# Kernel tuning notes

Hardware: AMD Instinct MI355X
Metric: run time of the kernel (lower is better)

Reference implementation:

```python
import jax, jax.numpy as jnp
import numpy as np
from jax import lax

DIM = 192
HEADS = 6

def conv1x1(x, w, b):
    # x: [B,C,H,W], w: [O,C], b: [O]
    return jnp.einsum('oc,bchw->bohw', w, x) + b[None, :, None, None]

def dwconv3x3(x, w, b):
    # x: [B,C,H,W], w: [C,1,3,3] depthwise
    y = lax.conv_general_dilated(x, w, window_strides=(1, 1), padding='SAME',
                                 feature_group_count=x.shape[1],
                                 dimension_numbers=('NCHW', 'OIHW', 'NCHW'))
    return y + b[None, :, None, None]

def l2norm(x, eps=1e-12):
    # normalize along last axis (matches torch F.normalize)
    n = jnp.sqrt(jnp.sum(x * x, axis=-1, keepdims=True))
    return x / jnp.maximum(n, eps)

def setup_inputs() -> dict:
    key = jax.random.key(0)
    ks = jax.random.split(key, 12)
    b, c, h, w = 8, DIM, 128, 128
    s = 0.02
    return {
        'hsi': jax.random.normal(ks[0], (b, c, h, w), jnp.float32),
        'lidar': jax.random.normal(ks[1], (b, c, h, w), jnp.float32),
        'hsi_qv_w': jax.random.normal(ks[2], (2 * c, c), jnp.float32) * s,
        'hsi_qv_b': jnp.zeros((2 * c,), jnp.float32),
        'lidar_kv_w': jax.random.normal(ks[3], (2 * c, c), jnp.float32) * s,
        'lidar_kv_b': jnp.zeros((2 * c,), jnp.float32),
        'hsi_dw_w': jax.random.normal(ks[4], (2 * c, 1, 3, 3), jnp.float32) * s,
        'hsi_dw_b': jnp.zeros((2 * c,), jnp.float32),
        'lidar_dw_w': jax.random.normal(ks[5], (2 * c, 1, 3, 3), jnp.float32) * s,
        'lidar_dw_b': jnp.zeros((2 * c,), jnp.float32),
        'temperature': jnp.ones((HEADS, 1, 1), jnp.float32),
    }

def reference(hsi, lidar, hsi_qv_w, hsi_qv_b, lidar_kv_w, lidar_kv_b,
              hsi_dw_w, hsi_dw_b, lidar_dw_w, lidar_dw_b, temperature):
    b, c, h, w = hsi.shape
    hd = c // HEADS  # per-head channel dim
    hw = h * w

    hsi_qv = dwconv3x3(conv1x1(hsi, hsi_qv_w, hsi_qv_b), hsi_dw_w, hsi_dw_b)
    hsi_q, hsi_v = jnp.split(hsi_qv, 2, axis=1)
    lidar_kv = dwconv3x3(conv1x1(lidar, lidar_kv_w, lidar_kv_b), lidar_dw_w, lidar_dw_b)
    lidar_k, lidar_v = jnp.split(lidar_kv, 2, axis=1)

    def to_heads(x):  # [B,C,H,W] -> [B,head,hd,HW]
        return x.reshape(b, HEADS, hd, hw)

    q = l2norm(to_heads(hsi_q))
    k = l2norm(to_heads(lidar_k))
    v_h = to_heads(hsi_v)
    v_l = to_heads(lidar_v)

    attn = jnp.einsum('bncs,bnds->bncd', q, k) * temperature[None]  # [B,head,hd,hd]
    attn = jax.nn.softmax(attn, axis=-1)  # dropout is identity in eval mode

    hsi_out = jnp.einsum('bncd,bnds->bncs', attn, v_h) + v_h
    lidar_out = jnp.einsum('bncd,bnds->bncs', attn, v_l) + v_l

    hsi_out = hsi_out.reshape(b, c, h, w) + hsi
    lidar_out = lidar_out.reshape(b, c, h, w) + lidar
    return (hsi_out, lidar_out)
```

## Files before the change

kernel.cpp:

```cpp
#include <hip/hip_runtime.h>

typedef short v8s __attribute__((ext_vector_type(8)));
typedef float v4f __attribute__((ext_vector_type(4)));
typedef float v32f __attribute__((ext_vector_type(32)));

__device__ __forceinline__ unsigned short f2bf(float f){
  unsigned u = __builtin_bit_cast(unsigned, f);
  return (unsigned short)((u + 0x7fffu + ((u>>16)&1u)) >> 16);
}
__device__ __forceinline__ float bf2f(unsigned short s){
  return __builtin_bit_cast(float, ((unsigned)s) << 16);
}

__global__ __launch_bounds__(512) void k_conv1x1(
    const float* __restrict__ hsi, const float* __restrict__ lidar,
    const unsigned short* __restrict__ Wfrag, const float* __restrict__ hqb,
    const float* __restrict__ lkb, unsigned short* __restrict__ S)
{
  const int bx   = blockIdx.x;
  const int tens = bx >> 11;
  const int nt   = bx & 2047;
  const int b    = nt >> 8;
  const int hw0  = (nt & 255) << 6;
  const float* X = (tens ? lidar : hsi) + ((size_t)b * 192) * 16384 + hw0;
  const float* bias = tens ? lkb : hqb;
  unsigned short* sb = S + ((size_t)(tens*8 + b) * 384) * 16384 + hw0;

  __shared__ unsigned short Xt[64][200];

  {
    const int c4   = (threadIdx.x & 15) * 4;
    const int krow = threadIdx.x >> 4;
    const float* xb2 = X + c4;
    float4 f[6];
    #pragma unroll
    for (int j = 0; j < 3; ++j){
      const int k = krow*2 + j*64;
      f[2*j]   = *(const float4*)(xb2 + (size_t)k * 16384);
      f[2*j+1] = *(const float4*)(xb2 + (size_t)(k+1) * 16384);
    }
    #pragma unroll
    for (int j = 0; j < 3; ++j){
      const int k = krow*2 + j*64;
      #pragma unroll
      for (int i2 = 0; i2 < 4; ++i2){
        const unsigned lo = f2bf(((const float*)&f[2*j])[i2]);
        const unsigned hi = f2bf(((const float*)&f[2*j+1])[i2]);
        *(unsigned*)&Xt[c4 + i2][k] = lo | (hi << 16);
      }
    }
  }
  __syncthreads();

  const int lane = threadIdx.x & 63;
  const int wid  = threadIdx.x >> 6;
  const int l15  = lane & 15;
  const int g    = lane >> 4;
  const int mstripe = wid * 48;
  const unsigned short* wb = Wfrag + ((size_t)(tens*8 + wid) * 18) * 512 + (lane << 3);

  v4f acc[3][4];
  #pragma unroll
  for (int i=0;i<3;i++)
    #pragma unroll
    for (int j=0;j<4;j++)
      acc[i][j] = (v4f){0.f,0.f,0.f,0.f};

  #pragma unroll
  for (int ks=0; ks<6; ++ks){
    const int k0 = ks*32;
    v8s af[3];
    #pragma unroll
    for (int mi=0; mi<3; ++mi)
      af[mi] = *(const v8s*)(wb + (size_t)(ks*3 + mi) * 512);
    #pragma unroll
    for (int ni=0; ni<4; ++ni){
      const v8s bfr = *(const v8s*)&Xt[ni*16 + l15][k0 + 8*g];
      #pragma unroll
      for (int mi=0; mi<3; ++mi)
        acc[mi][ni] = __builtin_amdgcn_mfma_f32_16x16x32_bf16(af[mi], bfr, acc[mi][ni], 0, 0, 0);
    }
  }

  #pragma unroll
  for (int mi=0; mi<3; ++mi){
    #pragma unroll
    for (int r=0; r<4; ++r){
      const int c = mstripe + mi*16 + 4*g + r;
      const float bs = bias[c];
      #pragma unroll
      for (int ni=0; ni<4; ++ni)
        sb[(size_t)c*16384 + ni*16 + l15] = f2bf(acc[mi][ni][r] + bs);
    }
  }
}

__global__ __launch_bounds__(256) void k_dw(
    const unsigned short* __restrict__ S, const float* __restrict__ hdw,
    const float* __restrict__ ldw, const float* __restrict__ hdb,
    const float* __restrict__ ldb, unsigned short* __restrict__ O)
{
  const int idx = blockIdx.x*256 + threadIdx.x;
  const int w8 = idx & 15;
  const int h  = (idx >> 4) & 127;
  const int bc = idx >> 11;
  const int c  = bc % 384;
  const int tens = (bc >= 3072);
  const unsigned short* in = S + (size_t)bc*16384;

  float r[3][10];
  #pragma unroll
  for (int dy=0; dy<3; ++dy){
    const int hh = h + dy - 1;
    if (hh >= 0 && hh < 128){
      const unsigned short* row = in + hh*128 + w8*8;
      const v8s m = *(const v8s*)row;
      #pragma unroll
      for (int i=0;i<8;++i) r[dy][i+1] = bf2f((unsigned short)m[i]);
      r[dy][0] = (w8 > 0)  ? bf2f(row[-1]) : 0.f;
      r[dy][9] = (w8 < 15) ? bf2f(row[8])  : 0.f;
    } else {
      #pragma unroll
      for (int i=0;i<10;++i) r[dy][i] = 0.f;
    }
  }
  const float* wp = (tens ? ldw : hdw) + c*9;
  const float k00=wp[0],k01=wp[1],k02=wp[2],k10=wp[3],k11=wp[4],k12=wp[5],k20=wp[6],k21=wp[7],k22=wp[8];
  const float bs = (tens ? ldb : hdb)[c];
  v8s out;
  #pragma unroll
  for (int j=0;j<8;++j){
    float a = bs
      + r[0][j]*k00 + r[0][j+1]*k01 + r[0][j+2]*k02
      + r[1][j]*k10 + r[1][j+1]*k11 + r[1][j+2]*k12
      + r[2][j]*k20 + r[2][j+1]*k21 + r[2][j+2]*k22;
    out[j] = (short)f2bf(a);
  }
  *(v8s*)(O + (size_t)bc*16384 + h*128 + w8*8) = out;
}

__global__ __launch_bounds__(256) void k_qk(
    const unsigned short* __restrict__ Q, const unsigned short* __restrict__ K,
    float* __restrict__ P)
{
  const int bh = blockIdx.x, split = blockIdx.y;
  const int lane = threadIdx.x & 63, wid = threadIdx.x >> 6;
  const int l15 = lane & 15, g = lane >> 4;
  const int b = bh/6, hd = bh%6;
  const unsigned short* qb = Q + ((size_t)b*384 + hd*32)*16384;
  const unsigned short* kb = K + ((size_t)b*384 + hd*32)*16384;
  const int s0 = (split*4 + wid)*256;

  v4f aqk[2][2], aqq[2], akk[2];
  #pragma unroll
  for (int i=0;i<2;i++){
    aqq[i] = (v4f){0.f,0.f,0.f,0.f};
    akk[i] = (v4f){0.f,0.f,0.f,0.f};
    #pragma unroll
    for (int j=0;j<2;j++) aqk[i][j] = (v4f){0.f,0.f,0.f,0.f};
  }

  #pragma unroll
  for (int ks=0; ks<8; ++ks){
    const int s = s0 + ks*32 + 8*g;
    v8s qf[2], kf[2];
    #pragma unroll
    for (int mi=0;mi<2;++mi) qf[mi] = *(const v8s*)(qb + (size_t)(mi*16 + l15)*16384 + s);
    #pragma unroll
    for (int ni=0;ni<2;++ni) kf[ni] = *(const v8s*)(kb + (size_t)(ni*16 + l15)*16384 + s);
    #pragma unroll
    for (int mi=0;mi<2;++mi)
      #pragma unroll
      for (int ni=0;ni<2;++ni)
        aqk[mi][ni] = __builtin_amdgcn_mfma_f32_16x16x32_bf16(qf[mi], kf[ni], aqk[mi][ni],0,0,0);
    #pragma unroll
    for (int mi=0;mi<2;++mi){
      aqq[mi] = __builtin_amdgcn_mfma_f32_16x16x32_bf16(qf[mi], qf[mi], aqq[mi],0,0,0);
      akk[mi] = __builtin_amdgcn_mfma_f32_16x16x32_bf16(kf[mi], kf[mi], akk[mi],0,0,0);
    }
  }
  float* slot = P + ((size_t)bh*64 + split*4 + wid)*1088;
  #pragma unroll
  for (int mi=0;mi<2;++mi)
    #pragma unroll
    for (int ni=0;ni<2;++ni)
      #pragma unroll
      for (int r=0;r<4;++r)
        slot[(mi*16 + 4*g + r)*32 + ni*16 + l15] = aqk[mi][ni][r];
  #pragma unroll
  for (int mi=0;mi<2;++mi)
    #pragma unroll
    for (int r=0;r<4;++r)
      if (l15 == 4*g + r){
        slot[1024 + mi*16 + l15] = aqq[mi][r];
        slot[1056 + mi*16 + l15] = akk[mi][r];
      }
}

__global__ __launch_bounds__(256) void k_sm(
    const float* __restrict__ P, const float* __restrict__ temp, float* __restrict__ A)
{
  __shared__ float red[1088];
  const int bh = blockIdx.x, t = threadIdx.x;
  const float* base = P + (size_t)bh*64*1088;
  for (int i=t; i<1088; i+=256){
    float s = 0.f;
    for (int sl=0; sl<64; ++sl) s += base[(size_t)sl*1088 + i];
    red[i] = s;
  }
  __syncthreads();
  const int c = t >> 3, dq = t & 7;
  const float qn = fmaxf(sqrtf(red[1024+c]), 1e-12f);
  const float tp = temp[bh % 6];
  float v[4];
  #pragma unroll
  for (int r=0;r<4;++r){
    const int d = dq*4 + r;
    const float kn = fmaxf(sqrtf(red[1056+d]), 1e-12f);
    v[r] = red[c*32+d] / (qn*kn) * tp;
  }
  float mx = fmaxf(fmaxf(v[0],v[1]), fmaxf(v[2],v[3]));
  mx = fmaxf(mx, __shfl_xor(mx,1));
  mx = fmaxf(mx, __shfl_xor(mx,2));
  mx = fmaxf(mx, __shfl_xor(mx,4));
  float e[4]; float sum = 0.f;
  #pragma unroll
  for (int r=0;r<4;++r){ e[r] = __expf(v[r]-mx); sum += e[r]; }
  sum += __shfl_xor(sum,1); sum += __shfl_xor(sum,2); sum += __shfl_xor(sum,4);
  const float inv = 1.f/sum;
  #pragma unroll
  for (int r=0;r<4;++r){
    const int d = dq*4 + r;
    A[(size_t)bh*1024 + c*32 + d] = e[r]*inv + ((c == d) ? 1.f : 0.f);
  }
}

#define R32(M) M(0) M(1) M(2) M(3) M(4) M(5) M(6) M(7) M(8) M(9) M(10) M(11) M(12) M(13) M(14) M(15) \
               M(16) M(17) M(18) M(19) M(20) M(21) M(22) M(23) M(24) M(25) M(26) M(27) M(28) M(29) M(30) M(31)

__global__ __launch_bounds__(256) void k_out(
    const float* __restrict__ A, const unsigned short* __restrict__ QVh,
    const unsigned short* __restrict__ KVl, const float* __restrict__ hsi,
    const float* __restrict__ lidar, float* __restrict__ outh, float* __restrict__ outl)
{
  const int tens = blockIdx.x & 1;
  const int bh = blockIdx.x >> 1;
  const int s = (blockIdx.y*256 + threadIdx.x)*2;
  const int b = bh/6, hd = bh%6;
  const float* Ab = A + (size_t)bh*1024;
  const unsigned short* V = (tens ? KVl : QVh) + ((size_t)b*384 + 192 + hd*32)*16384 + s;
  const float* X = (tens ? lidar : hsi) + ((size_t)b*192 + hd*32)*16384 + s;
  float* O = (tens ? outl : outh) + ((size_t)b*192 + hd*32)*16384 + s;

  v32f vx, vy;
#define LD_V(dd) { const unsigned u = *(const unsigned*)(V + (size_t)(dd)*16384); \
                   vx[dd] = bf2f((unsigned short)u); vy[dd] = bf2f((unsigned short)(u >> 16)); }
  R32(LD_V)
#undef LD_V

  for (int c=0; c<32; ++c){
    const float* Arow = Ab + c*32;
    const float2 x = *(const float2*)(X + (size_t)c*16384);
    float ax = x.x, ay = x.y;
#define FMA_D(dd) { const float a = Arow[dd]; ax += a*vx[dd]; ay += a*vy[dd]; }
    R32(FMA_D)
#undef FMA_D
    float2 o; o.x = ax; o.y = ay;
    *(float2*)(O + (size_t)c*16384) = o;
  }
}

__global__ __launch_bounds__(256) void k_wcvt(
    const float* __restrict__ a, const float* __restrict__ b, unsigned short* __restrict__ o)
{
  const int i = blockIdx.x*256 + threadIdx.x;
  if (i >= 147456) return;
  const int jj = i & 7;
  const int l  = (i >> 3) & 63;
  const int rest = i >> 9;
  const int mi = rest % 3;
  const int ks = (rest / 3) % 6;
  const int q  = rest / 18;
  const int wid = q & 7, tens = q >> 3;
  const int row = wid*48 + mi*16 + (l & 15);
  const int col = ks*32 + (l >> 4)*8 + jj;
  const float* src = tens ? b : a;
  o[i] = f2bf(src[row*192 + col]);
}

extern "C" void kernel_launch(void* const* d_in, const int* in_sizes, int n_in,
                              void* d_out, int out_size, void* d_ws, size_t ws_size,
                              hipStream_t stream) {
  const float* hsi   = (const float*)d_in[0];
  const float* lidar = (const float*)d_in[1];
  const float* hqw   = (const float*)d_in[2];
  const float* hqb   = (const float*)d_in[3];
  const float* lkw   = (const float*)d_in[4];
  const float* lkb   = (const float*)d_in[5];
  const float* hdw   = (const float*)d_in[6];
  const float* hdb   = (const float*)d_in[7];
  const float* ldw   = (const float*)d_in[8];
  const float* ldb   = (const float*)d_in[9];
  const float* temp  = (const float*)d_in[10];

  char* ws = (char*)d_ws;
  unsigned short* QVh = (unsigned short*)(ws);
  unsigned short* KVl = (unsigned short*)(ws + 100663296);
  unsigned short* Wbf = (unsigned short*)(ws + 201326592);
  float* P            = (float*)(ws + 201621504);
  float* A            = (float*)(ws + 214990848);

  float* outh = (float*)d_out;
  float* outl = outh + 25165824;
  unsigned short* S0 = (unsigned short*)d_out;

  k_wcvt<<<576, 256, 0, stream>>>(hqw, lkw, Wbf);
  k_conv1x1<<<4096, 512, 0, stream>>>(hsi, lidar, Wbf, hqb, lkb, S0);
  k_dw<<<49152, 256, 0, stream>>>(S0, hdw, ldw, hdb, ldb, QVh);
  k_qk<<<dim3(48, 16), 256, 0, stream>>>(QVh, KVl, P);
  k_sm<<<48, 256, 0, stream>>>(P, temp, A);
  k_out<<<dim3(96, 32), 256, 0, stream>>>(A, QVh, KVl, hsi, lidar, outh, outl);
}
```

Measured before the change: 383.2 us.

## Fuse V-half depthwise conv into output kernel, splitting QK and V buffers

The 1x1 conv output is split into a Q/K half and a V half. The standalone depthwise kernel now processes only the Q/K channels. The V-channel depthwise 3x3 is recomputed inside k_out from a haloed LDS tile, so the separate write and re-read of the convolved V tensor through global memory is gone. In exchange, k_out uses about 48KB of LDS per block and more registers, reads a 6-row halo for 4 output rows, and needs extra syncs.

```diff
diff --git a/kernel.cpp b/kernel.cpp
--- a/kernel.cpp
+++ b/kernel.cpp
@@ -15,7 +15,8 @@
 __global__ __launch_bounds__(512) void k_conv1x1(
     const float* __restrict__ hsi, const float* __restrict__ lidar,
     const unsigned short* __restrict__ Wfrag, const float* __restrict__ hqb,
-    const float* __restrict__ lkb, unsigned short* __restrict__ S)
+    const float* __restrict__ lkb, unsigned short* __restrict__ Sqk,
+    unsigned short* __restrict__ Sv)
 {
   const int bx   = blockIdx.x;
   const int tens = bx >> 11;
@@ -24,7 +25,6 @@
   const int hw0  = (nt & 255) << 6;
   const float* X = (tens ? lidar : hsi) + ((size_t)b * 192) * 16384 + hw0;
   const float* bias = tens ? lkb : hqb;
-  unsigned short* sb = S + ((size_t)(tens*8 + b) * 384) * 16384 + hw0;
 
   __shared__ unsigned short Xt[64][200];
 
@@ -82,31 +82,42 @@
     }
   }
 
+  unsigned short* outp;
+  int cb;
+  if (mstripe < 192){
+    outp = Sqk + ((size_t)(tens*8 + b) * 192) * 16384 + hw0;
+    cb = mstripe;
+  } else {
+    outp = Sv + ((size_t)(tens*8 + b) * 192) * 16384 + hw0;
+    cb = mstripe - 192;
+  }
   #pragma unroll
   for (int mi=0; mi<3; ++mi){
     #pragma unroll
     for (int r=0; r<4; ++r){
-      const int c = mstripe + mi*16 + 4*g + r;
-      const float bs = bias[c];
+      const int co = mi*16 + 4*g + r;
+      const float bs = bias[mstripe + co];
       #pragma unroll
       for (int ni=0; ni<4; ++ni)
-        sb[(size_t)c*16384 + ni*16 + l15] = f2bf(acc[mi][ni][r] + bs);
+        outp[(size_t)(cb + co)*16384 + ni*16 + l15] = f2bf(acc[mi][ni][r] + bs);
     }
   }
 }
 
 __global__ __launch_bounds__(256) void k_dw(
-    const unsigned short* __restrict__ S, const float* __restrict__ hdw,
+    const unsigned short* __restrict__ Sqk, const float* __restrict__ hdw,
     const float* __restrict__ ldw, const float* __restrict__ hdb,
-    const float* __restrict__ ldb, unsigned short* __restrict__ O)
+    const float* __restrict__ ldb, unsigned short* __restrict__ Qh,
+    unsigned short* __restrict__ Kl)
 {
   const int idx = blockIdx.x*256 + threadIdx.x;
   const int w8 = idx & 15;
   const int h  = (idx >> 4) & 127;
-  const int bc = idx >> 11;
-  const int c  = bc % 384;
-  const int tens = (bc >= 3072);
-  const unsigned short* in = S + (size_t)bc*16384;
+  const int pc = idx >> 11;
+  const int tens = (pc >= 1536);
+  const int lc = pc - tens*1536;
+  const int c  = lc % 192;
+  const unsigned short* in = Sqk + (size_t)pc*16384;
 
   float r[3][10];
   #pragma unroll
@@ -136,7 +147,7 @@
       + r[2][j]*k20 + r[2][j+1]*k21 + r[2][j+2]*k22;
     out[j] = (short)f2bf(a);
   }
-  *(v8s*)(O + (size_t)bc*16384 + h*128 + w8*8) = out;
+  *(v8s*)((tens ? Kl : Qh) + (size_t)lc*16384 + h*128 + w8*8) = out;
 }
 
 __global__ __launch_bounds__(256) void k_qk(
@@ -147,8 +158,8 @@
   const int lane = threadIdx.x & 63, wid = threadIdx.x >> 6;
   const int l15 = lane & 15, g = lane >> 4;
   const int b = bh/6, hd = bh%6;
-  const unsigned short* qb = Q + ((size_t)b*384 + hd*32)*16384;
-  const unsigned short* kb = K + ((size_t)b*384 + hd*32)*16384;
+  const unsigned short* qb = Q + ((size_t)b*192 + hd*32)*16384;
+  const unsigned short* kb = K + ((size_t)b*192 + hd*32)*16384;
   const int s0 = (split*4 + wid)*256;
 
   v4f aqk[2][2], aqq[2], akk[2];
@@ -239,21 +250,87 @@
                M(16) M(17) M(18) M(19) M(20) M(21) M(22) M(23) M(24) M(25) M(26) M(27) M(28) M(29) M(30) M(31)
 
 __global__ __launch_bounds__(256) void k_out(
-    const float* __restrict__ A, const unsigned short* __restrict__ QVh,
-    const unsigned short* __restrict__ KVl, const float* __restrict__ hsi,
-    const float* __restrict__ lidar, float* __restrict__ outh, float* __restrict__ outl)
+    const float* __restrict__ A, const unsigned short* __restrict__ Sv,
+    const float* __restrict__ hsi, const float* __restrict__ lidar,
+    const float* __restrict__ hdw, const float* __restrict__ ldw,
+    const float* __restrict__ hdb, const float* __restrict__ ldb,
+    float* __restrict__ outh, float* __restrict__ outl)
 {
   const int tens = blockIdx.x & 1;
-  const int bh = blockIdx.x >> 1;
-  const int s = (blockIdx.y*256 + threadIdx.x)*2;
+  const int bh   = blockIdx.x >> 1;
+  const int y    = blockIdx.y;
   const int b = bh/6, hd = bh%6;
+  const int t = threadIdx.x;
+
+  __shared__ __align__(16) unsigned short lds[24576];
+
+  {
+    const unsigned short* Sp = Sv + ((size_t)(tens*8 + b)*192 + hd*32)*16384;
+    #pragma unroll
+    for (int i=0;i<12;++i){
+      const int seg = i*256 + t;
+      const int ch  = seg / 96;
+      const int rem = seg % 96;
+      const int row = rem >> 4;
+      const int ws16= rem & 15;
+      const int grow = 4*y - 1 + row;
+      v8s val = (v8s){0,0,0,0,0,0,0,0};
+      if (grow >= 0 && grow < 128)
+        val = *(const v8s*)(Sp + (size_t)ch*16384 + grow*128 + ws16*8);
+      *(v8s*)&lds[(ch*6 + row)*128 + ws16*8] = val;
+    }
+  }
+  __syncthreads();
+
+  const int cg = t >> 6;
+  const int pg = t & 63;
+  const int rr = pg >> 4;
+  const int w0 = (pg & 15) * 8;
+  float vres[8][8];
+  const float* dwW = (tens ? ldw : hdw) + (192 + hd*32 + cg*8)*9;
+  const float* dwB = (tens ? ldb : hdb) + 192 + hd*32 + cg*8;
+  #pragma unroll
+  for (int cc=0; cc<8; ++cc){
+    const int ch = cg*8 + cc;
+    float a9[3][10];
+    #pragma unroll
+    for (int dy=0; dy<3; ++dy){
+      const unsigned short* rp = &lds[(ch*6 + rr + dy)*128];
+      const v8s m = *(const v8s*)(rp + w0);
+      #pragma unroll
+      for (int j=0;j<8;++j) a9[dy][j+1] = bf2f((unsigned short)m[j]);
+      a9[dy][0] = (w0 > 0)   ? bf2f(rp[w0-1]) : 0.f;
+      a9[dy][9] = (w0 < 120) ? bf2f(rp[w0+8]) : 0.f;
+    }
+    const float* wp = dwW + cc*9;
+    const float k00=wp[0],k01=wp[1],k02=wp[2],k10=wp[3],k11=wp[4],k12=wp[5],k20=wp[6],k21=wp[7],k22=wp[8];
+    const float bs = dwB[cc];
+    #pragma unroll
+    for (int j=0;j<8;++j)
+      vres[cc][j] = bs
+        + a9[0][j]*k00 + a9[0][j+1]*k01 + a9[0][j+2]*k02
+        + a9[1][j]*k10 + a9[1][j+1]*k11 + a9[1][j+2]*k12
+        + a9[2][j]*k20 + a9[2][j+1]*k21 + a9[2][j+2]*k22;
+  }
+  __syncthreads();
+
+  #pragma unroll
+  for (int cc=0; cc<8; ++cc){
+    v8s o;
+    #pragma unroll
+    for (int j=0;j<8;++j) o[j] = (short)f2bf(vres[cc][j]);
+    *(v8s*)&lds[(cg*8 + cc)*512 + pg*8] = o;
+  }
+  __syncthreads();
+
+  const int sl = 2*t;
+  const int s  = y*512 + sl;
   const float* Ab = A + (size_t)bh*1024;
-  const unsigned short* V = (tens ? KVl : QVh) + ((size_t)b*384 + 192 + hd*32)*16384 + s;
   const float* X = (tens ? lidar : hsi) + ((size_t)b*192 + hd*32)*16384 + s;
   float* O = (tens ? outl : outh) + ((size_t)b*192 + hd*32)*16384 + s;
 
   v32f vx, vy;
-#define LD_V(dd) { const unsigned u = *(const unsigned*)(V + (size_t)(dd)*16384); \
+#define LD_V(dd) { const unsigned u = *(const unsigned*)&lds[(dd)*512 + sl]; \
                    vx[dd] = bf2f((unsigned short)u); vy[dd] = bf2f((unsigned short)(u >> 16)); }
   R32(LD_V)
 #undef LD_V
@@ -304,20 +381,21 @@
   const float* temp  = (const float*)d_in[10];
 
   char* ws = (char*)d_ws;
-  unsigned short* QVh = (unsigned short*)(ws);
-  unsigned short* KVl = (unsigned short*)(ws + 100663296);
+  unsigned short* Sv  = (unsigned short*)(ws);
+  unsigned short* Qh  = (unsigned short*)(ws + 100663296);
+  unsigned short* Kl  = (unsigned short*)(ws + 150994944);
   unsigned short* Wbf = (unsigned short*)(ws + 201326592);
   float* P            = (float*)(ws + 201621504);
   float* A            = (float*)(ws + 214990848);
 
   float* outh = (float*)d_out;
   float* outl = outh + 25165824;
-  unsigned short* S0 = (unsigned short*)d_out;
+  unsigned short* Sqk = (unsigned short*)d_out;
 
   k_wcvt<<<576, 256, 0, stream>>>(hqw, lkw, Wbf);
-  k_conv1x1<<<4096, 512, 0, stream>>>(hsi, lidar, Wbf, hqb, lkb, S0);
-  k_dw<<<49152, 256, 0, stream>>>(S0, hdw, ldw, hdb, ldb, QVh);
-  k_qk<<<dim3(48, 16), 256, 0, stream>>>(QVh, KVl, P);
+  k_conv1x1<<<4096, 512, 0, stream>>>(hsi, lidar, Wbf, hqb, lkb, Sqk, Sv);
+  k_dw<<<24576, 256, 0, stream>>>(Sqk, hdw, ldw, hdb, ldb, Qh, Kl);
+  k_qk<<<dim3(48, 16), 256, 0, stream>>>(Qh, Kl, P);
   k_sm<<<48, 256, 0, stream>>>(P, temp, A);
-  k_out<<<dim3(96, 32), 256, 0, stream>>>(A, QVh, KVl, hsi, lidar, outh, outl);
-}
+  k_out<<<dim3(96, 32), 256, 0, stream>>>(A, Sv, hsi, lidar, hdw, ldw, hdb, ldb, outh, outl);
+}
```

New measurement: 497.0 us. +29.7%, slower.

## Split QK/V intermediates into separate buffers and stage depthwise conv rows in LDS

Applied to the files above, without the earlier changes.

The 1x1 conv now writes its q/k channels and its v channels into two separate bf16 buffers, one placed in the output region and one in workspace. The depthwise conv kernel is rewritten to load an 18-row halo tile into shared memory once per 16-row block, so each thread no longer fetches three overlapping global rows plus scalar edge elements. Downstream kernels index the new QK and V buffers directly. This is meant to cut redundant global reads and uncoalesced edge loads in the depthwise stage, at the cost of more buffer aliasing inside d_out and an added barrier per block.

```diff
diff --git a/kernel.cpp b/kernel.cpp
--- a/kernel.cpp
+++ b/kernel.cpp
@@ -15,7 +15,8 @@
 __global__ __launch_bounds__(512) void k_conv1x1(
     const float* __restrict__ hsi, const float* __restrict__ lidar,
     const unsigned short* __restrict__ Wfrag, const float* __restrict__ hqb,
-    const float* __restrict__ lkb, unsigned short* __restrict__ S)
+    const float* __restrict__ lkb, unsigned short* __restrict__ Sqk,
+    unsigned short* __restrict__ Sv)
 {
   const int bx   = blockIdx.x;
   const int tens = bx >> 11;
@@ -24,7 +25,6 @@
   const int hw0  = (nt & 255) << 6;
   const float* X = (tens ? lidar : hsi) + ((size_t)b * 192) * 16384 + hw0;
   const float* bias = tens ? lkb : hqb;
-  unsigned short* sb = S + ((size_t)(tens*8 + b) * 384) * 16384 + hw0;
 
   __shared__ unsigned short Xt[64][200];
 
@@ -82,73 +82,103 @@
     }
   }
 
+  unsigned short* outp;
+  int cb;
+  if (mstripe < 192){
+    outp = Sqk + ((size_t)(tens*8 + b) * 192) * 16384 + hw0;
+    cb = mstripe;
+  } else {
+    outp = Sv + ((size_t)(tens*8 + b) * 192) * 16384 + hw0;
+    cb = mstripe - 192;
+  }
   #pragma unroll
   for (int mi=0; mi<3; ++mi){
     #pragma unroll
     for (int r=0; r<4; ++r){
-      const int c = mstripe + mi*16 + 4*g + r;
-      const float bs = bias[c];
+      const int co = mi*16 + 4*g + r;
+      const float bs = bias[mstripe + co];
       #pragma unroll
       for (int ni=0; ni<4; ++ni)
-        sb[(size_t)c*16384 + ni*16 + l15] = f2bf(acc[mi][ni][r] + bs);
-    }
-  }
-}
-
-__global__ __launch_bounds__(256) void k_dw(
-    const unsigned short* __restrict__ S, const float* __restrict__ hdw,
-    const float* __restrict__ ldw, const float* __restrict__ hdb,
-    const float* __restrict__ ldb, unsigned short* __restrict__ O)
-{
-  const int idx = blockIdx.x*256 + threadIdx.x;
-  const int w8 = idx & 15;
-  const int h  = (idx >> 4) & 127;
-  const int bc = idx >> 11;
-  const int c  = bc % 384;
-  const int tens = (bc >= 3072);
-  const unsigned short* in = S + (size_t)bc*16384;
-
-  float r[3][10];
+        outp[(size_t)(cb + co)*16384 + ni*16 + l15] = f2bf(acc[mi][ni][r] + bs);
+    }
+  }
+}
+
+__global__ __launch_bounds__(256) void k_dw2(
+    const unsigned short* __restrict__ Sqk, const unsigned short* __restrict__ Sv,
+    const float* __restrict__ hdw, const float* __restrict__ ldw,
+    const float* __restrict__ hdb, const float* __restrict__ ldb,
+    unsigned short* __restrict__ QKd, unsigned short* __restrict__ Vb)
+{
+  const int bx = blockIdx.x;
+  const int ytile = bx & 7;
+  const int gp = bx >> 3;
+  const int half = (gp >= 3072);
+  const int p = half ? gp - 3072 : gp;
+  const int tens = (p >= 1536);
+  const int c = p % 192;
+  const int woff = half ? 192 : 0;
+  const unsigned short* in = (half ? Sv : Sqk) + (size_t)p*16384;
+  unsigned short* out = (half ? Vb : QKd) + (size_t)p*16384;
+  const int h0 = ytile*16;
+  const int t = threadIdx.x;
+
+  __shared__ __align__(16) unsigned short lds[18*136];
+
+  #pragma unroll
+  for (int it=0; it<2; ++it){
+    const int slot = it*256 + t;
+    if (slot < 288){
+      const int row = slot >> 4;
+      const int w16 = slot & 15;
+      const int gr = h0 - 1 + row;
+      v8s val = (v8s){0,0,0,0,0,0,0,0};
+      if (gr >= 0 && gr < 128)
+        val = *(const v8s*)(in + gr*128 + w16*8);
+      *(v8s*)&lds[row*136 + w16*8] = val;
+    }
+  }
+  __syncthreads();
+
+  const int w8 = t & 15;
+  const int hr = t >> 4;
+  const int w0 = w8*8;
+
+  float a9[3][10];
   #pragma unroll
   for (int dy=0; dy<3; ++dy){
-    const int hh = h + dy - 1;
-    if (hh >= 0 && hh < 128){
-      const unsigned short* row = in + hh*128 + w8*8;
-      const v8s m = *(const v8s*)row;
-      #pragma unroll
-      for (int i=0;i<8;++i) r[dy][i+1] = bf2f((unsigned short)m[i]);
-      r[dy][0] = (w8 > 0)  ? bf2f(row[-1]) : 0.f;
-      r[dy][9] = (w8 < 15) ? bf2f(row[8])  : 0.f;
-    } else {
-      #pragma unroll
-      for (int i=0;i<10;++i) r[dy][i] = 0.f;
-    }
-  }
-  const float* wp = (tens ? ldw : hdw) + c*9;
+    const unsigned short* rp = &lds[(hr + dy)*136];
+    const v8s m = *(const v8s*)(rp + w0);
+    #pragma unroll
+    for (int j=0;j<8;++j) a9[dy][j+1] = bf2f((unsigned short)m[j]);
+    a9[dy][0] = (w8 > 0)  ? bf2f(rp[w0-1]) : 0.f;
+    a9[dy][9] = (w8 < 15) ? bf2f(rp[w0+8]) : 0.f;
+  }
+
+  const float* wp = (tens ? ldw : hdw) + (woff + c)*9;
   const float k00=wp[0],k01=wp[1],k02=wp[2],k10=wp[3],k11=wp[4],k12=wp[5],k20=wp[6],k21=wp[7],k22=wp[8];
-  const float bs = (tens ? ldb : hdb)[c];
-  v8s out;
+  const float bs = (tens ? ldb : hdb)[woff + c];
+  v8s o;
   #pragma unroll
   for (int j=0;j<8;++j){
     float a = bs
-      + r[0][j]*k00 + r[0][j+1]*k01 + r[0][j+2]*k02
-      + r[1][j]*k10 + r[1][j+1]*k11 + r[1][j+2]*k12
-      + r[2][j]*k20 + r[2][j+1]*k21 + r[2][j+2]*k22;
-    out[j] = (short)f2bf(a);
-  }
-  *(v8s*)(O + (size_t)bc*16384 + h*128 + w8*8) = out;
+      + a9[0][j]*k00 + a9[0][j+1]*k01 + a9[0][j+2]*k02
+      + a9[1][j]*k10 + a9[1][j+1]*k11 + a9[1][j+2]*k12
+      + a9[2][j]*k20 + a9[2][j+1]*k21 + a9[2][j+2]*k22;
+    o[j] = (short)f2bf(a);
+  }
+  *(v8s*)(out + (h0 + hr)*128 + w0) = o;
 }
 
 __global__ __launch_bounds__(256) void k_qk(
-    const unsigned short* __restrict__ Q, const unsigned short* __restrict__ K,
-    float* __restrict__ P)
+    const unsigned short* __restrict__ QKd, float* __restrict__ P)
 {
   const int bh = blockIdx.x, split = blockIdx.y;
   const int lane = threadIdx.x & 63, wid = threadIdx.x >> 6;
   const int l15 = lane & 15, g = lane >> 4;
   const int b = bh/6, hd = bh%6;
-  const unsigned short* qb = Q + ((size_t)b*384 + hd*32)*16384;
-  const unsigned short* kb = K + ((size_t)b*384 + hd*32)*16384;
+  const unsigned short* qb = QKd + ((size_t)(0*8 + b)*192 + hd*32)*16384;
+  const unsigned short* kb = QKd + ((size_t)(1*8 + b)*192 + hd*32)*16384;
   const int s0 = (split*4 + wid)*256;
 
   v4f aqk[2][2], aqq[2], akk[2];
@@ -239,16 +269,16 @@
                M(16) M(17) M(18) M(19) M(20) M(21) M(22) M(23) M(24) M(25) M(26) M(27) M(28) M(29) M(30) M(31)
 
 __global__ __launch_bounds__(256) void k_out(
-    const float* __restrict__ A, const unsigned short* __restrict__ QVh,
-    const unsigned short* __restrict__ KVl, const float* __restrict__ hsi,
-    const float* __restrict__ lidar, float* __restrict__ outh, float* __restrict__ outl)
+    const float* __restrict__ A, const unsigned short* __restrict__ Vb,
+    const float* __restrict__ hsi, const float* __restrict__ lidar,
+    float* __restrict__ outh, float* __restrict__ outl)
 {
   const int tens = blockIdx.x & 1;
   const int bh = blockIdx.x >> 1;
   const int s = (blockIdx.y*256 + threadIdx.x)*2;
   const int b = bh/6, hd = bh%6;
   const float* Ab = A + (size_t)bh*1024;
-  const unsigned short* V = (tens ? KVl : QVh) + ((size_t)b*384 + 192 + hd*32)*16384 + s;
+  const unsigned short* V = Vb + ((size_t)(tens*8 + b)*192 + hd*32)*16384 + s;
   const float* X = (tens ? lidar : hsi) + ((size_t)b*192 + hd*32)*16384 + s;
   float* O = (tens ? outl : outh) + ((size_t)b*192 + hd*32)*16384 + s;
 
@@ -304,20 +334,21 @@
   const float* temp  = (const float*)d_in[10];
 
   char* ws = (char*)d_ws;
-  unsigned short* QVh = (unsigned short*)(ws);
-  unsigned short* KVl = (unsigned short*)(ws + 100663296);
+  unsigned short* Sv  = (unsigned short*)(ws);
+  unsigned short* Vb  = (unsigned short*)(ws + 100663296);
   unsigned short* Wbf = (unsigned short*)(ws + 201326592);
   float* P            = (float*)(ws + 201621504);
   float* A            = (float*)(ws + 214990848);
 
   float* outh = (float*)d_out;
   float* outl = outh + 25165824;
-  unsigned short* S0 = (unsigned short*)d_out;
+  unsigned short* Sqk = (unsigned short*)d_out;
+  unsigned short* QKd = (unsigned short*)((char*)d_out + 100663296);
 
   k_wcvt<<<576, 256, 0, stream>>>(hqw, lkw, Wbf);
-  k_conv1x1<<<4096, 512, 0, stream>>>(hsi, lidar, Wbf, hqb, lkb, S0);
-  k_dw<<<49152, 256, 0, stream>>>(S0, hdw, ldw, hdb, ldb, QVh);
-  k_qk<<<dim3(48, 16), 256, 0, stream>>>(QVh, KVl, P);
+  k_conv1x1<<<4096, 512, 0, stream>>>(hsi, lidar, Wbf, hqb, lkb, Sqk, Sv);
+  k_dw2<<<49152, 256, 0, stream>>>(Sqk, Sv, hdw, ldw, hdb, ldb, QKd, Vb);
+  k_qk<<<dim3(48, 16), 256, 0, stream>>>(QKd, P);
   k_sm<<<48, 256, 0, stream>>>(P, temp, A);
-  k_out<<<dim3(96, 32), 256, 0, stream>>>(A, QVh, KVl, hsi, lidar, outh, outl);
-}
+  k_out<<<dim3(96, 32), 256, 0, stream>>>(A, Vb, hsi, lidar, outh, outl);
+}
```

New measurement: 339.3 us (median of 2 runs). -11.4%, faster.
